# Performance work log

Measured on AMD Instinct MI355X. Metric: run time of the kernel, lower is better.

The kernel has to match this reference:

```python
import jax, jax.numpy as jnp
import numpy as np

T, D, N, W = 8192, 768, 10000, 32  # tokens, hidden dim, num spans, max span width


def setup_inputs() -> dict:
    key = jax.random.key(0)
    k1, k2, k3, k4, k5 = jax.random.split(key, 5)
    sentence_embeddings = jax.random.normal(k1, (T, D), dtype=jnp.float32)
    lengths = jax.random.randint(k2, (N,), 1, W + 1)           # span lengths in [1, W]
    starts = jax.random.randint(k3, (N,), 0, T - W)
    ends = starts + lengths - 1                                 # inclusive end, < T
    sentence_spans = jnp.stack([starts, ends], axis=1).astype(jnp.int32)
    Wq = (jax.random.normal(k4, (D, D), dtype=jnp.float32) / np.sqrt(D).astype(np.float32))
    bq = jax.random.normal(k5, (D,), dtype=jnp.float32) * 0.01
    return {"sentence_embeddings": sentence_embeddings,
            "sentence_spans": sentence_spans,
            "Wq": Wq, "bq": bq}


def reference(sentence_embeddings, sentence_spans, Wq, bq):
    # Padded + masked batched version of the per-span loop:
    #   span_emb = emb[s:e+1]; q = span_emb @ Wq.T + bq
    #   w = softmax(q @ span_emb.T, dim=1); out = (w @ span_emb).sum(0)
    starts = sentence_spans[:, 0]                               # [N]
    lengths = sentence_spans[:, 1] - starts + 1                 # inclusive end -> length
    offs = jnp.arange(W)
    pos = starts[:, None] + offs[None, :]                       # [N, W] token indices
    valid = offs[None, :] < lengths[:, None]                    # [N, W] in-span mask
    pos = jnp.clip(pos, 0, sentence_embeddings.shape[0] - 1)
    span_emb = sentence_embeddings[pos]                         # [N, W, D] ragged gather
    span_emb = jnp.where(valid[:, :, None], span_emb, 0.0)
    query = jnp.einsum('nwd,ed->nwe', span_emb, Wq) + bq        # [N, W, D]
    scores = jnp.einsum('nqd,nkd->nqk', query, span_emb)        # [N, W, W]
    scores = jnp.where(valid[:, None, :], scores, -jnp.inf)     # mask pad keys (softmax dim=1)
    weights = jax.nn.softmax(scores, axis=-1)
    attn = jnp.einsum('nqk,nkd->nqd', weights, span_emb)        # [N, W, D]
    attn = jnp.where(valid[:, :, None], attn, 0.0)              # drop pad query rows
    return attn.sum(axis=1)                                     # [N, D] == torch.sum(attention, dim=0) per span
```

## Files before the change

### kernel.cpp

```cpp
#include <hip/hip_runtime.h>
#include <hip/hip_bf16.h>
#include <cstddef>
#include <cstdint>

constexpr int Tt = 8192;
constexpr int Dd = 768;
constexpr int Nn = 10000;
constexpr int Ww = 32;

typedef __bf16 bf16x8 __attribute__((ext_vector_type(8)));
typedef __bf16 bf16x4 __attribute__((ext_vector_type(4)));
typedef _Float16 half8v __attribute__((ext_vector_type(8)));
typedef _Float16 half4v __attribute__((ext_vector_type(4)));
typedef float f32x4 __attribute__((ext_vector_type(4)));

#define MFMA16(a, b, c) __builtin_amdgcn_mfma_f32_16x16x32_bf16((a), (b), (c), 0, 0, 0)
#define MFMAH(a, b, c) __builtin_amdgcn_mfma_f32_16x16x32_f16((a), (b), (c), 0, 0, 0)

__global__ __launch_bounds__(256) void conv_f16_kernel(const float* __restrict__ emb,
                                                       const float* __restrict__ Wq,
                                                       _Float16* __restrict__ Ef,
                                                       _Float16* __restrict__ Wf) {
    const int nE = (Tt * Dd) / 4;
    const int nW = (Dd * Dd) / 4;
    const int i = blockIdx.x * 256 + threadIdx.x;
    if (i < nE) {
        const float4 v = reinterpret_cast<const float4*>(emb)[i];
        half4v o;
        o[0] = (_Float16)v.x; o[1] = (_Float16)v.y;
        o[2] = (_Float16)v.z; o[3] = (_Float16)v.w;
        reinterpret_cast<half4v*>(Ef)[i] = o;
    } else {
        const int j = i - nE;
        if (j < nW) {
            const float4 v = reinterpret_cast<const float4*>(Wq)[j];
            half4v o;
            o[0] = (_Float16)v.x; o[1] = (_Float16)v.y;
            o[2] = (_Float16)v.z; o[3] = (_Float16)v.w;
            reinterpret_cast<half4v*>(Wf)[j] = o;
        }
    }
}

template <bool LO>
__global__ __launch_bounds__(256) void conv_kernel(const float* __restrict__ src,
                                                   __bf16* __restrict__ h,
                                                   __bf16* __restrict__ l, int n4) {
    const int i = blockIdx.x * 256 + threadIdx.x;
    if (i >= n4) return;
    const float4 v = reinterpret_cast<const float4*>(src)[i];
    bf16x4 oh, ol;
    oh[0] = (__bf16)v.x; oh[1] = (__bf16)v.y; oh[2] = (__bf16)v.z; oh[3] = (__bf16)v.w;
    reinterpret_cast<bf16x4*>(h)[i] = oh;
    if (LO) {
        ol[0] = (__bf16)(v.x - (float)oh[0]);
        ol[1] = (__bf16)(v.y - (float)oh[1]);
        ol[2] = (__bf16)(v.z - (float)oh[2]);
        ol[3] = (__bf16)(v.w - (float)oh[3]);
        reinterpret_cast<bf16x4*>(l)[i] = ol;
    }
}

__global__ __launch_bounds__(256) void zero_kernel(int* __restrict__ p, int n) {
    const int i = blockIdx.x * 256 + threadIdx.x;
    if (i < n) p[i] = 0;
}

__global__ __launch_bounds__(256) void hist_kernel(const int* __restrict__ spans,
                                                   int* __restrict__ hist) {
    const int i = blockIdx.x * 256 + threadIdx.x;
    if (i < Nn) atomicAdd(&hist[spans[2 * i]], 1);
}

__global__ __launch_bounds__(256) void scan_kernel(int* __restrict__ hist) {
    __shared__ int part[256];
    const int t = threadIdx.x;
    int vals[32];
    int sum = 0;
#pragma unroll
    for (int i = 0; i < 32; ++i) { vals[i] = hist[t * 32 + i]; sum += vals[i]; }
    part[t] = sum;
    __syncthreads();
    for (int off = 1; off < 256; off <<= 1) {
        const int v = (t >= off) ? part[t - off] : 0;
        __syncthreads();
        part[t] += v;
        __syncthreads();
    }
    int run = (t == 0) ? 0 : part[t - 1];
#pragma unroll
    for (int i = 0; i < 32; ++i) { const int v = vals[i]; hist[t * 32 + i] = run; run += v; }
}

__global__ __launch_bounds__(256) void scatter_kernel(const int* __restrict__ spans,
                                                      int* __restrict__ offs,
                                                      int* __restrict__ perm) {
    const int i = blockIdx.x * 256 + threadIdx.x;
    if (i < Nn) {
        const int p = atomicAdd(&offs[spans[2 * i]], 1);
        perm[p] = i;
    }
}

template <bool SPLIT>
__global__ __launch_bounds__(256) void qproj_kernel(const float* __restrict__ emb,
                                                    const float* __restrict__ Wq,
                                                    const float* __restrict__ bq,
                                                    __bf16* __restrict__ Qh,
                                                    __bf16* __restrict__ Ql) {
    __shared__ float As[64][32];
    __shared__ float Bs[64][32];
    const int tid = threadIdx.x;
    const int tx = tid & 15;
    const int ty = tid >> 4;
    const int m0 = blockIdx.x * 64;
    const int n0 = blockIdx.y * 64;

    float acc[4][4] = {};

    for (int kc = 0; kc < Dd; kc += 32) {
#pragma unroll
        for (int i = 0; i < 2; ++i) {
            const int f   = tid + i * 256;
            const int row = f >> 3;
            const int c4  = f & 7;
            const int ph  = (c4 + (row >> 2)) & 7;
            *reinterpret_cast<float4*>(&As[row][ph * 4]) =
                *reinterpret_cast<const float4*>(&emb[(size_t)(m0 + row) * Dd + kc + c4 * 4]);
            *reinterpret_cast<float4*>(&Bs[row][ph * 4]) =
                *reinterpret_cast<const float4*>(&Wq[(size_t)(n0 + row) * Dd + kc + c4 * 4]);
        }
        __syncthreads();
#pragma unroll
        for (int d4 = 0; d4 < 8; ++d4) {
            float4 av[4], bv[4];
#pragma unroll
            for (int r = 0; r < 4; ++r)
                av[r] = *reinterpret_cast<const float4*>(&As[ty * 4 + r][((d4 + ty) & 7) * 4]);
#pragma unroll
            for (int c = 0; c < 4; ++c)
                bv[c] = *reinterpret_cast<const float4*>(&Bs[tx * 4 + c][((d4 + tx) & 7) * 4]);
#pragma unroll
            for (int r = 0; r < 4; ++r)
#pragma unroll
                for (int c = 0; c < 4; ++c) {
                    acc[r][c] += av[r].x * bv[c].x;
                    acc[r][c] += av[r].y * bv[c].y;
                    acc[r][c] += av[r].z * bv[c].z;
                    acc[r][c] += av[r].w * bv[c].w;
                }
        }
        __syncthreads();
    }
#pragma unroll
    for (int r = 0; r < 4; ++r) {
        bf16x4 oh, ol;
#pragma unroll
        for (int c = 0; c < 4; ++c) {
            const float v = acc[r][c] + bq[n0 + tx * 4 + c];
            const __bf16 h = (__bf16)v;
            oh[c] = h;
            if (SPLIT) ol[c] = (__bf16)(v - (float)h);
        }
        const size_t off = (size_t)(m0 + ty * 4 + r) * Dd + n0 + tx * 4;
        *reinterpret_cast<bf16x4*>(&Qh[off]) = oh;
        if (SPLIT) *reinterpret_cast<bf16x4*>(&Ql[off]) = ol;
    }
}

__global__ __launch_bounds__(256) void qproj_f16_kernel(const _Float16* __restrict__ Ef,
                                                        const _Float16* __restrict__ Wf,
                                                        const float* __restrict__ bq,
                                                        _Float16* __restrict__ Qf) {
    __shared__ __align__(16) _Float16 As[128 * 64];
    __shared__ __align__(16) _Float16 Bs[96 * 64];

    const int tid  = threadIdx.x;
    const int wave = tid >> 6;
    const int lane = tid & 63;

    const int b   = blockIdx.x;
    const int xcd = b & 7;
    const int li  = b >> 3;
    const int mt  = xcd * 8 + (li >> 3);
    const int nt  = li & 7;
    const int m0 = mt * 128;
    const int n0 = nt * 96;
    const int wm = (wave & 1) * 64;
    const int wn = (wave >> 1) * 48;
    const int fr = lane & 15;
    const int kg = lane >> 4;

    int ar[4], ao[4];
#pragma unroll
    for (int i = 0; i < 4; ++i) {
        const int s = tid + i * 256;
        ar[i] = s >> 3;
        ao[i] = ((s & 7) ^ (ar[i] & 7)) * 8;
    }
    int br[3], bo[3];
#pragma unroll
    for (int i = 0; i < 3; ++i) {
        const int s = tid + i * 256;
        br[i] = s >> 3;
        bo[i] = ((s & 7) ^ (br[i] & 7)) * 8;
    }

    f32x4 acc[4][3] = {};

    for (int kc = 0; kc < Dd; kc += 64) {
        half8v ra[4], rb[3];
#pragma unroll
        for (int i = 0; i < 4; ++i)
            ra[i] = *reinterpret_cast<const half8v*>(&Ef[(size_t)(m0 + ar[i]) * Dd + kc + ao[i]]);
#pragma unroll
        for (int i = 0; i < 3; ++i)
            rb[i] = *reinterpret_cast<const half8v*>(&Wf[(size_t)(n0 + br[i]) * Dd + kc + bo[i]]);
        __syncthreads();
#pragma unroll
        for (int i = 0; i < 4; ++i)
            *reinterpret_cast<half8v*>(&As[(tid + i * 256) * 8]) = ra[i];
#pragma unroll
        for (int i = 0; i < 3; ++i)
            *reinterpret_cast<half8v*>(&Bs[(tid + i * 256) * 8]) = rb[i];
        __syncthreads();

#pragma unroll
        for (int step = 0; step < 2; ++step) {
            const int g = kg + 4 * step;
            half8v a[4], bb[3];
#pragma unroll
            for (int r = 0; r < 4; ++r) {
                const int R = wm + r * 16 + fr;
                a[r] = *reinterpret_cast<const half8v*>(&As[R * 64 + (g ^ (R & 7)) * 8]);
            }
#pragma unroll
            for (int c = 0; c < 3; ++c) {
                const int R = wn + c * 16 + fr;
                bb[c] = *reinterpret_cast<const half8v*>(&Bs[R * 64 + (g ^ (R & 7)) * 8]);
            }
#pragma unroll
            for (int r = 0; r < 4; ++r)
#pragma unroll
                for (int c = 0; c < 3; ++c)
                    acc[r][c] = MFMAH(a[r], bb[c], acc[r][c]);
        }
    }

#pragma unroll
    for (int c = 0; c < 3; ++c) {
        const int ocol = n0 + wn + c * 16 + fr;
        const float bqv = bq[ocol];
#pragma unroll
        for (int r = 0; r < 4; ++r)
#pragma unroll
            for (int j = 0; j < 4; ++j) {
                const int orow = m0 + wm + r * 16 + kg * 4 + j;
                Qf[(size_t)orow * Dd + ocol] = (_Float16)(acc[r][c][j] + bqv);
            }
    }
}

__global__ __launch_bounds__(256) void span_attn_win_kernel(const _Float16* __restrict__ Ef,
                                                            const int* __restrict__ spans,
                                                            const _Float16* __restrict__ Qf,
                                                            const int* __restrict__ perm,
                                                            float* __restrict__ out) {
    constexpr int WR = 48, CH = 128, ST = 136, NCH = Dd / CH;
    __shared__ __align__(16) _Float16 Qs[WR * ST];
    __shared__ __align__(16) _Float16 Es[WR * ST];

    const int tid  = threadIdx.x;
    const int wave = tid >> 6;
    const int lane = tid & 63;

    const int b     = blockIdx.x;
    const int bp    = (b & 7) * 313 + (b >> 3);
    const int slot0 = bp * 4;
    const int slot  = slot0 + wave;
    const bool active = slot < Nn;

    int s0 = perm[slot0 < Nn ? slot0 : (Nn - 1)];
    if ((unsigned)s0 >= (unsigned)Nn) s0 = 0;
    int s = active ? perm[slot] : s0;
    if ((unsigned)s >= (unsigned)Nn) s = 0;

    const int w0    = spans[2 * s0];
    const int start = spans[2 * s];
    const int L     = spans[2 * s + 1] - start + 1;
    const bool big  = L > 16;
    const int sl    = start - w0;
    const bool inwin = active && sl >= 0 && sl <= (WR - 32);

    const int row = lane & 15;
    const int kq  = lane >> 4;

    const size_t gq = (size_t)(start + row) * Dd + kq * 8;

    f32x4 acc00 = {0.f, 0.f, 0.f, 0.f};
    f32x4 acc01 = {0.f, 0.f, 0.f, 0.f};
    f32x4 acc10 = {0.f, 0.f, 0.f, 0.f};
    f32x4 acc11 = {0.f, 0.f, 0.f, 0.f};

    for (int c = 0; c < NCH; ++c) {
        const int c0 = c * CH;
        __syncthreads();
#pragma unroll
        for (int i = 0; i < 3; ++i) {
            const int seg = tid + i * 256;
            const int r  = seg >> 4;
            const int cs = seg & 15;
            const int gr = w0 + r < Tt ? w0 + r : Tt - 1;
            const size_t ga = (size_t)gr * Dd + c0 + cs * 8;
            *reinterpret_cast<half8v*>(&Qs[r * ST + cs * 8]) =
                *reinterpret_cast<const half8v*>(&Qf[ga]);
            *reinterpret_cast<half8v*>(&Es[r * ST + cs * 8]) =
                *reinterpret_cast<const half8v*>(&Ef[ga]);
        }
        __syncthreads();

        if (inwin) {
            const int ab = (sl + row) * ST + kq * 8;
#pragma unroll
            for (int j = 0; j < 4; ++j) {
                const int o = j * 32;
                const half8v a0 = *reinterpret_cast<const half8v*>(&Qs[ab + o]);
                const half8v b0 = *reinterpret_cast<const half8v*>(&Es[ab + o]);
                acc00 = MFMAH(a0, b0, acc00);
                if (big) {
                    const half8v a1 = *reinterpret_cast<const half8v*>(&Qs[ab + 16 * ST + o]);
                    const half8v b1 = *reinterpret_cast<const half8v*>(&Es[ab + 16 * ST + o]);
                    acc01 = MFMAH(a0, b1, acc01);
                    acc10 = MFMAH(a1, b0, acc10);
                    acc11 = MFMAH(a1, b1, acc11);
                }
            }
        } else if (active) {
#pragma unroll
            for (int j = 0; j < 4; ++j) {
                const int o = c0 + j * 32;
                const half8v a0 = *reinterpret_cast<const half8v*>(&Qf[gq + o]);
                const half8v b0 = *reinterpret_cast<const half8v*>(&Ef[gq + o]);
                acc00 = MFMAH(a0, b0, acc00);
                if (big) {
                    const half8v a1 = *reinterpret_cast<const half8v*>(&Qf[gq + 16 * Dd + o]);
                    const half8v b1 = *reinterpret_cast<const half8v*>(&Ef[gq + 16 * Dd + o]);
                    acc01 = MFMAH(a0, b1, acc01);
                    acc10 = MFMAH(a1, b0, acc10);
                    acc11 = MFMAH(a1, b1, acc11);
                }
            }
        }
    }

    const float NEG = -1e30f;
    const bool kv0 = row < L;
    const bool kv1 = (16 + row) < L;
    float cA, cB;
    {
        float w00[4], w01[4], w10[4], w11[4];
#pragma unroll
        for (int r = 0; r < 4; ++r) {
            float m = kv0 ? acc00[r] : NEG;
            if (big) m = fmaxf(m, kv1 ? acc01[r] : NEG);
#pragma unroll
            for (int st = 1; st <= 8; st <<= 1) m = fmaxf(m, __shfl_xor(m, st));
            const float e0 = kv0 ? __expf(acc00[r] - m) : 0.f;
            const float e1 = (big && kv1) ? __expf(acc01[r] - m) : 0.f;
            float sum = e0 + e1;
#pragma unroll
            for (int st = 1; st <= 8; st <<= 1) sum += __shfl_xor(sum, st);
            const float inv = 1.f / sum;
            const bool qv = (kq * 4 + r) < L;
            w00[r] = qv ? e0 * inv : 0.f;
            w01[r] = qv ? e1 * inv : 0.f;
            if (big) {
                float mh = kv0 ? acc10[r] : NEG;
                mh = fmaxf(mh, kv1 ? acc11[r] : NEG);
#pragma unroll
                for (int st = 1; st <= 8; st <<= 1) mh = fmaxf(mh, __shfl_xor(mh, st));
                const float f0 = kv0 ? __expf(acc10[r] - mh) : 0.f;
                const float f1 = kv1 ? __expf(acc11[r] - mh) : 0.f;
                float sh = f0 + f1;
#pragma unroll
                for (int st = 1; st <= 8; st <<= 1) sh += __shfl_xor(sh, st);
                const float invh = 1.f / sh;
                const bool qvh = (16 + kq * 4 + r) < L;
                w10[r] = qvh ? f0 * invh : 0.f;
                w11[r] = qvh ? f1 * invh : 0.f;
            }
        }
        float pa = w00[0] + w00[1] + w00[2] + w00[3];
        float pb = 0.f;
        if (big) {
            pa += w10[0] + w10[1] + w10[2] + w10[3];
            pb = w01[0] + w01[1] + w01[2] + w01[3] +
                 w11[0] + w11[1] + w11[2] + w11[3];
        }
        pa += __shfl_xor(pa, 16);
        pa += __shfl_xor(pa, 32);
        if (big) {
            pb += __shfl_xor(pb, 16);
            pb += __shfl_xor(pb, 32);
        }
        cA = pa;
        cB = pb;
    }

    if (active) {
        f32x4 o[3] = {};
        const int KP = (L + 3) & ~3;
        const _Float16* ebase = Ef + (size_t)start * Dd + lane * 4;
        for (int k = 0; k < KP; k += 4) {
            float cv[4];
            half4v ev[4][3];
#pragma unroll
            for (int j = 0; j < 4; ++j) {
                const int kk = k + j;
                cv[j] = (kk < 16) ? __shfl(cA, kk) : __shfl(cB, kk - 16);
#pragma unroll
                for (int i = 0; i < 3; ++i)
                    ev[j][i] = *reinterpret_cast<const half4v*>(ebase + (size_t)kk * Dd + i * 256);
            }
#pragma unroll
            for (int j = 0; j < 4; ++j)
#pragma unroll
                for (int i = 0; i < 3; ++i) {
                    o[i][0] += cv[j] * (float)ev[j][i][0];
                    o[i][1] += cv[j] * (float)ev[j][i][1];
                    o[i][2] += cv[j] * (float)ev[j][i][2];
                    o[i][3] += cv[j] * (float)ev[j][i][3];
                }
        }
#pragma unroll
        for (int i = 0; i < 3; ++i)
            *reinterpret_cast<f32x4*>(&out[(size_t)s * Dd + i * 256 + lane * 4]) = o[i];
    }
}

template <bool SPLIT, bool SORTED>
__global__ __launch_bounds__(256) void span_attn_g_kernel(const __bf16* __restrict__ Eb,
                                                          const int* __restrict__ spans,
                                                          const __bf16* __restrict__ Qh,
                                                          const __bf16* __restrict__ Ql,
                                                          const int* __restrict__ perm,
                                                          float* __restrict__ out) {
    const int wave = threadIdx.x >> 6;
    const int lane = threadIdx.x & 63;

    int s;
    bool active;
    if (SORTED) {
        const int b    = blockIdx.x;
        const int bp   = (b & 7) * 313 + (b >> 3);
        const int slot = bp * 4 + wave;
        active = slot < Nn;
        int sv = active ? perm[slot] : 0;
        if ((unsigned)sv >= (unsigned)Nn) sv = 0;
        s = sv;
    } else {
        s = blockIdx.x * 4 + wave;
        active = true;
    }

    const int start = spans[2 * s];
    const int L     = spans[2 * s + 1] - start + 1;
    const bool big  = L > 16;

    const int row = lane & 15;
    const int kq  = lane >> 4;

    const size_t rbase = (size_t)(start + row) * Dd + kq * 8;
    const __bf16* qh0 = Qh + rbase;
    const __bf16* eb0 = Eb + rbase;
    const __bf16* ql0 = SPLIT ? (Ql + rbase) : nullptr;

    f32x4 acc00 = {0.f, 0.f, 0.f, 0.f};
    f32x4 acc01 = {0.f, 0.f, 0.f, 0.f};
    f32x4 acc10 = {0.f, 0.f, 0.f, 0.f};
    f32x4 acc11 = {0.f, 0.f, 0.f, 0.f};

    if (!big) {
        for (int kc = 0; kc < Dd; kc += 128) {
            bf16x8 A[4], B[4], AL[4];
#pragma unroll
            for (int j = 0; j < 4; ++j) {
                const int o = kc + j * 32;
                A[j] = *reinterpret_cast<const bf16x8*>(qh0 + o);
                B[j] = *reinterpret_cast<const bf16x8*>(eb0 + o);
                if (SPLIT) AL[j] = *reinterpret_cast<const bf16x8*>(ql0 + o);
            }
#pragma unroll
            for (int j = 0; j < 4; ++j) {
                acc00 = MFMA16(A[j], B[j], acc00);
                if (SPLIT) acc00 = MFMA16(AL[j], B[j], acc00);
            }
        }
    } else {
        for (int kc = 0; kc < Dd; kc += 64) {
            bf16x8 A0[2], A1[2], B0[2], B1[2], AL0[2], AL1[2];
#pragma unroll
            for (int j = 0; j < 2; ++j) {
                const int o = kc + j * 32;
                A0[j] = *reinterpret_cast<const bf16x8*>(qh0 + o);
                A1[j] = *reinterpret_cast<const bf16x8*>(qh0 + 16 * Dd + o);
                B0[j] = *reinterpret_cast<const bf16x8*>(eb0 + o);
                B1[j] = *reinterpret_cast<const bf16x8*>(eb0 + 16 * Dd + o);
                if (SPLIT) {
                    AL0[j] = *reinterpret_cast<const bf16x8*>(ql0 + o);
                    AL1[j] = *reinterpret_cast<const bf16x8*>(ql0 + 16 * Dd + o);
                }
            }
#pragma unroll
            for (int j = 0; j < 2; ++j) {
                acc00 = MFMA16(A0[j], B0[j], acc00);
                acc01 = MFMA16(A0[j], B1[j], acc01);
                acc10 = MFMA16(A1[j], B0[j], acc10);
                acc11 = MFMA16(A1[j], B1[j], acc11);
                if (SPLIT) {
                    acc00 = MFMA16(AL0[j], B0[j], acc00);
                    acc01 = MFMA16(AL0[j], B1[j], acc01);
                    acc10 = MFMA16(AL1[j], B0[j], acc10);
                    acc11 = MFMA16(AL1[j], B1[j], acc11);
                }
            }
        }
    }

    const float NEG = -1e30f;
    const bool kv0 = row < L;
    const bool kv1 = (16 + row) < L;
    float cA, cB;
    {
        float w00[4], w01[4], w10[4], w11[4];
#pragma unroll
        for (int r = 0; r < 4; ++r) {
            float m = kv0 ? acc00[r] : NEG;
            if (big) m = fmaxf(m, kv1 ? acc01[r] : NEG);
#pragma unroll
            for (int st = 1; st <= 8; st <<= 1) m = fmaxf(m, __shfl_xor(m, st));
            const float e0 = kv0 ? __expf(acc00[r] - m) : 0.f;
            const float e1 = (big && kv1) ? __expf(acc01[r] - m) : 0.f;
            float sum = e0 + e1;
#pragma unroll
            for (int st = 1; st <= 8; st <<= 1) sum += __shfl_xor(sum, st);
            const float inv = 1.f / sum;
            const bool qv = (kq * 4 + r) < L;
            w00[r] = qv ? e0 * inv : 0.f;
            w01[r] = qv ? e1 * inv : 0.f;
            if (big) {
                float mh = kv0 ? acc10[r] : NEG;
                mh = fmaxf(mh, kv1 ? acc11[r] : NEG);
#pragma unroll
                for (int st = 1; st <= 8; st <<= 1) mh = fmaxf(mh, __shfl_xor(mh, st));
                const float f0 = kv0 ? __expf(acc10[r] - mh) : 0.f;
                const float f1 = kv1 ? __expf(acc11[r] - mh) : 0.f;
                float sh = f0 + f1;
#pragma unroll
                for (int st = 1; st <= 8; st <<= 1) sh += __shfl_xor(sh, st);
                const float invh = 1.f / sh;
                const bool qvh = (16 + kq * 4 + r) < L;
                w10[r] = qvh ? f0 * invh : 0.f;
                w11[r] = qvh ? f1 * invh : 0.f;
            }
        }
        float pa = w00[0] + w00[1] + w00[2] + w00[3];
        float pb = 0.f;
        if (big) {
            pa += w10[0] + w10[1] + w10[2] + w10[3];
            pb = w01[0] + w01[1] + w01[2] + w01[3] +
                 w11[0] + w11[1] + w11[2] + w11[3];
        }
        pa += __shfl_xor(pa, 16);
        pa += __shfl_xor(pa, 32);
        if (big) {
            pb += __shfl_xor(pb, 16);
            pb += __shfl_xor(pb, 32);
        }
        cA = pa;
        cB = pb;
    }

    if (active) {
        f32x4 o[3] = {};
        const int KP = (L + 3) & ~3;
        const __bf16* ebase = Eb + (size_t)start * Dd + lane * 4;
        for (int k = 0; k < KP; k += 4) {
            float cv[4];
            bf16x4 ev[4][3];
#pragma unroll
            for (int j = 0; j < 4; ++j) {
                const int kk = k + j;
                cv[j] = (kk < 16) ? __shfl(cA, kk) : __shfl(cB, kk - 16);
#pragma unroll
                for (int i = 0; i < 3; ++i)
                    ev[j][i] = *reinterpret_cast<const bf16x4*>(ebase + (size_t)kk * Dd + i * 256);
            }
#pragma unroll
            for (int j = 0; j < 4; ++j)
#pragma unroll
                for (int i = 0; i < 3; ++i) {
                    o[i][0] += cv[j] * (float)ev[j][i][0];
                    o[i][1] += cv[j] * (float)ev[j][i][1];
                    o[i][2] += cv[j] * (float)ev[j][i][2];
                    o[i][3] += cv[j] * (float)ev[j][i][3];
                }
        }
#pragma unroll
        for (int i = 0; i < 3; ++i)
            *reinterpret_cast<f32x4*>(&out[(size_t)s * Dd + i * 256 + lane * 4]) = o[i];
    }
}

extern "C" void kernel_launch(void* const* d_in, const int* in_sizes, int n_in,
                              void* d_out, int out_size, void* d_ws, size_t ws_size,
                              hipStream_t stream) {
    const float* emb   = (const float*)d_in[0];
    const int*   spans = (const int*)d_in[1];
    const float* Wq    = (const float*)d_in[2];
    const float* bq    = (const float*)d_in[3];
    float*       out   = (float*)d_out;

    const size_t TD = (size_t)Tt * Dd;
    const size_t DD = (size_t)Dd * Dd;
    const size_t intBytes = (size_t)(8192 + 10016) * sizeof(int);
    auto align16 = [](size_t x) { return (x + 15) & ~(size_t)15; };

    const size_t needMain = align16((2 * TD + DD) * 2) + intBytes;
    const size_t needB = align16(3 * TD * 2) + intBytes;
    const size_t needC = 3 * TD * 2;

    if (ws_size >= needMain) {
        char* base = (char*)d_ws;
        _Float16* Qf = (_Float16*)base;
        _Float16* Ef = (_Float16*)(base + TD * 2);
        _Float16* Wf = (_Float16*)(base + 2 * TD * 2);
        int* hist = (int*)(base + align16((2 * TD + DD) * 2));
        int* perm = hist + 8192;

        const int convBlocks = (int)((TD / 4 + DD / 4) / 256);
        conv_f16_kernel<<<convBlocks, 256, 0, stream>>>(emb, Wq, Ef, Wf);
        zero_kernel<<<32, 256, 0, stream>>>(hist, 8192);
        hist_kernel<<<40, 256, 0, stream>>>(spans, hist);
        scan_kernel<<<1, 256, 0, stream>>>(hist);
        scatter_kernel<<<40, 256, 0, stream>>>(spans, hist, perm);
        qproj_f16_kernel<<<512, 256, 0, stream>>>(Ef, Wf, bq, Qf);
        span_attn_win_kernel<<<2504, 256, 0, stream>>>(Ef, spans, Qf, perm, out);
    } else if (ws_size >= needB) {
        __bf16* w = (__bf16*)d_ws;
        __bf16* Qh = w;
        __bf16* Ql = w + TD;
        __bf16* Eh = w + 2 * TD;
        int* hist = (int*)((char*)d_ws + align16(3 * TD * 2));
        int* perm = hist + 8192;

        conv_kernel<false><<<(int)(TD / 4 / 256), 256, 0, stream>>>(emb, Eh, nullptr, (int)(TD / 4));
        zero_kernel<<<32, 256, 0, stream>>>(hist, 8192);
        hist_kernel<<<40, 256, 0, stream>>>(spans, hist);
        scan_kernel<<<1, 256, 0, stream>>>(hist);
        scatter_kernel<<<40, 256, 0, stream>>>(spans, hist, perm);
        qproj_kernel<true><<<dim3(Tt / 64, Dd / 64), 256, 0, stream>>>(emb, Wq, bq, Qh, Ql);
        span_attn_g_kernel<true, true><<<2504, 256, 0, stream>>>(Eh, spans, Qh, Ql, perm, out);
    } else if (ws_size >= needC) {
        __bf16* w = (__bf16*)d_ws;
        __bf16* Qh = w;
        __bf16* Ql = w + TD;
        __bf16* Eh = w + 2 * TD;
        conv_kernel<false><<<(int)(TD / 4 / 256), 256, 0, stream>>>(emb, Eh, nullptr, (int)(TD / 4));
        qproj_kernel<true><<<dim3(Tt / 64, Dd / 64), 256, 0, stream>>>(emb, Wq, bq, Qh, Ql);
        span_attn_g_kernel<true, false><<<2500, 256, 0, stream>>>(Eh, spans, Qh, Ql, nullptr, out);
    } else {
        __bf16* w = (__bf16*)d_ws;
        __bf16* Qh = w;
        __bf16* Eh = w + TD;
        conv_kernel<false><<<(int)(TD / 4 / 256), 256, 0, stream>>>(emb, Eh, nullptr, (int)(TD / 4));
        qproj_kernel<false><<<dim3(Tt / 64, Dd / 64), 256, 0, stream>>>(emb, Wq, bq, Qh, nullptr);
        span_attn_g_kernel<false, false><<<2500, 256, 0, stream>>>(Eh, spans, Qh, nullptr, nullptr, out);
    }
}
```

Measured before the change: 152.6 us.

## Process two sorted spans per wave and register-prefetch next window chunk

Each block now handles 8 sorted spans (two per wave) instead of 4, so each shared-memory window of Q and E rows is reused by more spans, and the grid is halved to 1250 blocks with a new XCD-aware block remap. The next 128-column chunk is loaded into registers while the current chunk is being consumed, which overlaps global loads with MFMA work. The cost is more registers per thread (two accumulator sets plus prefetch buffers) and fewer blocks, which may lower occupancy and parallelism. The active guard was also removed, so correctness relies on 1250*8 exactly covering N.

```diff
diff --git a/kernel.cpp b/kernel.cpp
--- a/kernel.cpp
+++ b/kernel.cpp
@@ -274,167 +274,199 @@
     const int wave = tid >> 6;
     const int lane = tid & 63;
 
-    const int b     = blockIdx.x;
-    const int bp    = (b & 7) * 313 + (b >> 3);
-    const int slot0 = bp * 4;
-    const int slot  = slot0 + wave;
-    const bool active = slot < Nn;
-
-    int s0 = perm[slot0 < Nn ? slot0 : (Nn - 1)];
+    const int b   = blockIdx.x;
+    const int xcd = b & 7;
+    const int li  = b >> 3;
+    const int bp  = (xcd < 2) ? xcd * 157 + li : 314 + (xcd - 2) * 156 + li;
+    const int slot0 = bp * 8;
+
+    int s0 = perm[slot0];
     if ((unsigned)s0 >= (unsigned)Nn) s0 = 0;
-    int s = active ? perm[slot] : s0;
-    if ((unsigned)s >= (unsigned)Nn) s = 0;
-
-    const int w0    = spans[2 * s0];
-    const int start = spans[2 * s];
-    const int L     = spans[2 * s + 1] - start + 1;
-    const bool big  = L > 16;
-    const int sl    = start - w0;
-    const bool inwin = active && sl >= 0 && sl <= (WR - 32);
+    const int w0 = spans[2 * s0];
 
     const int row = lane & 15;
     const int kq  = lane >> 4;
 
-    const size_t gq = (size_t)(start + row) * Dd + kq * 8;
-
-    f32x4 acc00 = {0.f, 0.f, 0.f, 0.f};
-    f32x4 acc01 = {0.f, 0.f, 0.f, 0.f};
-    f32x4 acc10 = {0.f, 0.f, 0.f, 0.f};
-    f32x4 acc11 = {0.f, 0.f, 0.f, 0.f};
+    int  sS[2], stS[2], LS[2];
+    bool bigS[2], inwS[2];
+#pragma unroll
+    for (int sp = 0; sp < 2; ++sp) {
+        int s = perm[slot0 + wave * 2 + sp];
+        if ((unsigned)s >= (unsigned)Nn) s = 0;
+        sS[sp]   = s;
+        stS[sp]  = spans[2 * s];
+        LS[sp]   = spans[2 * s + 1] - stS[sp] + 1;
+        bigS[sp] = LS[sp] > 16;
+        const int sl = stS[sp] - w0;
+        inwS[sp] = (sl >= 0) && (sl <= (WR - 32));
+    }
+
+    int    ldso[3];
+    size_t gbo[3];
+#pragma unroll
+    for (int i = 0; i < 3; ++i) {
+        const int seg = tid + i * 256;
+        const int r   = seg >> 4;
+        const int cs  = seg & 15;
+        ldso[i] = r * ST + cs * 8;
+        const int gr = (w0 + r < Tt) ? (w0 + r) : (Tt - 1);
+        gbo[i] = (size_t)gr * Dd + cs * 8;
+    }
+
+    f32x4 acc[2][4] = {};
+
+    half8v rq[3], re[3];
+#pragma unroll
+    for (int i = 0; i < 3; ++i) {
+        rq[i] = *reinterpret_cast<const half8v*>(&Qf[gbo[i]]);
+        re[i] = *reinterpret_cast<const half8v*>(&Ef[gbo[i]]);
+    }
 
     for (int c = 0; c < NCH; ++c) {
+        __syncthreads();
+#pragma unroll
+        for (int i = 0; i < 3; ++i) {
+            *reinterpret_cast<half8v*>(&Qs[ldso[i]]) = rq[i];
+            *reinterpret_cast<half8v*>(&Es[ldso[i]]) = re[i];
+        }
+        __syncthreads();
+
+        if (c + 1 < NCH) {
+            const size_t cb = (size_t)(c + 1) * CH;
+#pragma unroll
+            for (int i = 0; i < 3; ++i) {
+                rq[i] = *reinterpret_cast<const half8v*>(&Qf[gbo[i] + cb]);
+                re[i] = *reinterpret_cast<const half8v*>(&Ef[gbo[i] + cb]);
+            }
+        }
+
         const int c0 = c * CH;
-        __syncthreads();
-#pragma unroll
-        for (int i = 0; i < 3; ++i) {
-            const int seg = tid + i * 256;
-            const int r  = seg >> 4;
-            const int cs = seg & 15;
-            const int gr = w0 + r < Tt ? w0 + r : Tt - 1;
-            const size_t ga = (size_t)gr * Dd + c0 + cs * 8;
-            *reinterpret_cast<half8v*>(&Qs[r * ST + cs * 8]) =
-                *reinterpret_cast<const half8v*>(&Qf[ga]);
-            *reinterpret_cast<half8v*>(&Es[r * ST + cs * 8]) =
-                *reinterpret_cast<const half8v*>(&Ef[ga]);
-        }
-        __syncthreads();
-
-        if (inwin) {
-            const int ab = (sl + row) * ST + kq * 8;
-#pragma unroll
-            for (int j = 0; j < 4; ++j) {
-                const int o = j * 32;
-                const half8v a0 = *reinterpret_cast<const half8v*>(&Qs[ab + o]);
-                const half8v b0 = *reinterpret_cast<const half8v*>(&Es[ab + o]);
-                acc00 = MFMAH(a0, b0, acc00);
+#pragma unroll
+        for (int sp = 0; sp < 2; ++sp) {
+            const bool big = bigS[sp];
+            if (inwS[sp]) {
+                const int ab = (stS[sp] - w0 + row) * ST + kq * 8;
+#pragma unroll
+                for (int j = 0; j < 4; ++j) {
+                    const int o = j * 32;
+                    const half8v a0 = *reinterpret_cast<const half8v*>(&Qs[ab + o]);
+                    const half8v b0 = *reinterpret_cast<const half8v*>(&Es[ab + o]);
+                    acc[sp][0] = MFMAH(a0, b0, acc[sp][0]);
+                    if (big) {
+                        const half8v a1 = *reinterpret_cast<const half8v*>(&Qs[ab + 16 * ST + o]);
+                        const half8v b1 = *reinterpret_cast<const half8v*>(&Es[ab + 16 * ST + o]);
+                        acc[sp][1] = MFMAH(a0, b1, acc[sp][1]);
+                        acc[sp][2] = MFMAH(a1, b0, acc[sp][2]);
+                        acc[sp][3] = MFMAH(a1, b1, acc[sp][3]);
+                    }
+                }
+            } else {
+                const size_t gq = (size_t)(stS[sp] + row) * Dd + kq * 8;
+#pragma unroll
+                for (int j = 0; j < 4; ++j) {
+                    const int o = c0 + j * 32;
+                    const half8v a0 = *reinterpret_cast<const half8v*>(&Qf[gq + o]);
+                    const half8v b0 = *reinterpret_cast<const half8v*>(&Ef[gq + o]);
+                    acc[sp][0] = MFMAH(a0, b0, acc[sp][0]);
+                    if (big) {
+                        const half8v a1 = *reinterpret_cast<const half8v*>(&Qf[gq + 16 * Dd + o]);
+                        const half8v b1 = *reinterpret_cast<const half8v*>(&Ef[gq + 16 * Dd + o]);
+                        acc[sp][1] = MFMAH(a0, b1, acc[sp][1]);
+                        acc[sp][2] = MFMAH(a1, b0, acc[sp][2]);
+                        acc[sp][3] = MFMAH(a1, b1, acc[sp][3]);
+                    }
+                }
+            }
+        }
+    }
+
+#pragma unroll
+    for (int sp = 0; sp < 2; ++sp) {
+        const int  L   = LS[sp];
+        const bool big = bigS[sp];
+        const float NEG = -1e30f;
+        const bool kv0 = row < L;
+        const bool kv1 = (16 + row) < L;
+        float cA, cB;
+        {
+            float w00[4], w01[4], w10[4], w11[4];
+#pragma unroll
+            for (int r = 0; r < 4; ++r) {
+                float m = kv0 ? acc[sp][0][r] : NEG;
+                if (big) m = fmaxf(m, kv1 ? acc[sp][1][r] : NEG);
+#pragma unroll
+                for (int st = 1; st <= 8; st <<= 1) m = fmaxf(m, __shfl_xor(m, st));
+                const float e0 = kv0 ? __expf(acc[sp][0][r] - m) : 0.f;
+                const float e1 = (big && kv1) ? __expf(acc[sp][1][r] - m) : 0.f;
+                float sum = e0 + e1;
+#pragma unroll
+                for (int st = 1; st <= 8; st <<= 1) sum += __shfl_xor(sum, st);
+                const float inv = 1.f / sum;
+                const bool qv = (kq * 4 + r) < L;
+                w00[r] = qv ? e0 * inv : 0.f;
+                w01[r] = qv ? e1 * inv : 0.f;
                 if (big) {
-                    const half8v a1 = *reinterpret_cast<const half8v*>(&Qs[ab + 16 * ST + o]);
-                    const half8v b1 = *reinterpret_cast<const half8v*>(&Es[ab + 16 * ST + o]);
-                    acc01 = MFMAH(a0, b1, acc01);
-                    acc10 = MFMAH(a1, b0, acc10);
-                    acc11 = MFMAH(a1, b1, acc11);
+                    float mh = kv0 ? acc[sp][2][r] : NEG;
+                    mh = fmaxf(mh, kv1 ? acc[sp][3][r] : NEG);
+#pragma unroll
+                    for (int st = 1; st <= 8; st <<= 1) mh = fmaxf(mh, __shfl_xor(mh, st));
+                    const float f0 = kv0 ? __expf(acc[sp][2][r] - mh) : 0.f;
+                    const float f1 = kv1 ? __expf(acc[sp][3][r] - mh) : 0.f;
+                    float sh = f0 + f1;
+#pragma unroll
+                    for (int st = 1; st <= 8; st <<= 1) sh += __shfl_xor(sh, st);
+                    const float invh = 1.f / sh;
+                    const bool qvh = (16 + kq * 4 + r) < L;
+                    w10[r] = qvh ? f0 * invh : 0.f;
+                    w11[r] = qvh ? f1 * invh : 0.f;
                 }
             }
-        } else if (active) {
-#pragma unroll
-            for (int j = 0; j < 4; ++j) {
-                const int o = c0 + j * 32;
-                const half8v a0 = *reinterpret_cast<const half8v*>(&Qf[gq + o]);
-                const half8v b0 = *reinterpret_cast<const half8v*>(&Ef[gq + o]);
-                acc00 = MFMAH(a0, b0, acc00);
-                if (big) {
-                    const half8v a1 = *reinterpret_cast<const half8v*>(&Qf[gq + 16 * Dd + o]);
-                    const half8v b1 = *reinterpret_cast<const half8v*>(&Ef[gq + 16 * Dd + o]);
-                    acc01 = MFMAH(a0, b1, acc01);
-                    acc10 = MFMAH(a1, b0, acc10);
-                    acc11 = MFMAH(a1, b1, acc11);
+            float pa = w00[0] + w00[1] + w00[2] + w00[3];
+            float pb = 0.f;
+            if (big) {
+                pa += w10[0] + w10[1] + w10[2] + w10[3];
+                pb = w01[0] + w01[1] + w01[2] + w01[3] +
+                     w11[0] + w11[1] + w11[2] + w11[3];
+            }
+            pa += __shfl_xor(pa, 16);
+            pa += __shfl_xor(pa, 32);
+            if (big) {
+                pb += __shfl_xor(pb, 16);
+                pb += __shfl_xor(pb, 32);
+            }
+            cA = pa;
+            cB = pb;
+        }
+
+        {
+            f32x4 o[3] = {};
+            const int KP = (L + 3) & ~3;
+            const _Float16* ebase = Ef + (size_t)stS[sp] * Dd + lane * 4;
+            for (int k = 0; k < KP; k += 4) {
+                float cv[4];
+                half4v ev[4][3];
+#pragma unroll
+                for (int j = 0; j < 4; ++j) {
+                    const int kk = k + j;
+                    cv[j] = (kk < 16) ? __shfl(cA, kk) : __shfl(cB, kk - 16);
+#pragma unroll
+                    for (int i = 0; i < 3; ++i)
+                        ev[j][i] = *reinterpret_cast<const half4v*>(ebase + (size_t)kk * Dd + i * 256);
                 }
-            }
-        }
-    }
-
-    const float NEG = -1e30f;
-    const bool kv0 = row < L;
-    const bool kv1 = (16 + row) < L;
-    float cA, cB;
-    {
-        float w00[4], w01[4], w10[4], w11[4];
-#pragma unroll
-        for (int r = 0; r < 4; ++r) {
-            float m = kv0 ? acc00[r] : NEG;
-            if (big) m = fmaxf(m, kv1 ? acc01[r] : NEG);
-#pragma unroll
-            for (int st = 1; st <= 8; st <<= 1) m = fmaxf(m, __shfl_xor(m, st));
-            const float e0 = kv0 ? __expf(acc00[r] - m) : 0.f;
-            const float e1 = (big && kv1) ? __expf(acc01[r] - m) : 0.f;
-            float sum = e0 + e1;
-#pragma unroll
-            for (int st = 1; st <= 8; st <<= 1) sum += __shfl_xor(sum, st);
-            const float inv = 1.f / sum;
-            const bool qv = (kq * 4 + r) < L;
-            w00[r] = qv ? e0 * inv : 0.f;
-            w01[r] = qv ? e1 * inv : 0.f;
-            if (big) {
-                float mh = kv0 ? acc10[r] : NEG;
-                mh = fmaxf(mh, kv1 ? acc11[r] : NEG);
-#pragma unroll
-                for (int st = 1; st <= 8; st <<= 1) mh = fmaxf(mh, __shfl_xor(mh, st));
-                const float f0 = kv0 ? __expf(acc10[r] - mh) : 0.f;
-                const float f1 = kv1 ? __expf(acc11[r] - mh) : 0.f;
-                float sh = f0 + f1;
-#pragma unroll
-                for (int st = 1; st <= 8; st <<= 1) sh += __shfl_xor(sh, st);
-                const float invh = 1.f / sh;
-                const bool qvh = (16 + kq * 4 + r) < L;
-                w10[r] = qvh ? f0 * invh : 0.f;
-                w11[r] = qvh ? f1 * invh : 0.f;
-            }
-        }
-        float pa = w00[0] + w00[1] + w00[2] + w00[3];
-        float pb = 0.f;
-        if (big) {
-            pa += w10[0] + w10[1] + w10[2] + w10[3];
-            pb = w01[0] + w01[1] + w01[2] + w01[3] +
-                 w11[0] + w11[1] + w11[2] + w11[3];
-        }
-        pa += __shfl_xor(pa, 16);
-        pa += __shfl_xor(pa, 32);
-        if (big) {
-            pb += __shfl_xor(pb, 16);
-            pb += __shfl_xor(pb, 32);
-        }
-        cA = pa;
-        cB = pb;
-    }
-
-    if (active) {
-        f32x4 o[3] = {};
-        const int KP = (L + 3) & ~3;
-        const _Float16* ebase = Ef + (size_t)start * Dd + lane * 4;
-        for (int k = 0; k < KP; k += 4) {
-            float cv[4];
-            half4v ev[4][3];
-#pragma unroll
-            for (int j = 0; j < 4; ++j) {
-                const int kk = k + j;
-                cv[j] = (kk < 16) ? __shfl(cA, kk) : __shfl(cB, kk - 16);
-#pragma unroll
-                for (int i = 0; i < 3; ++i)
-                    ev[j][i] = *reinterpret_cast<const half4v*>(ebase + (size_t)kk * Dd + i * 256);
-            }
-#pragma unroll
-            for (int j = 0; j < 4; ++j)
-#pragma unroll
-                for (int i = 0; i < 3; ++i) {
-                    o[i][0] += cv[j] * (float)ev[j][i][0];
-                    o[i][1] += cv[j] * (float)ev[j][i][1];
-                    o[i][2] += cv[j] * (float)ev[j][i][2];
-                    o[i][3] += cv[j] * (float)ev[j][i][3];
-                }
-        }
-#pragma unroll
-        for (int i = 0; i < 3; ++i)
-            *reinterpret_cast<f32x4*>(&out[(size_t)s * Dd + i * 256 + lane * 4]) = o[i];
+#pragma unroll
+                for (int j = 0; j < 4; ++j)
+#pragma unroll
+                    for (int i = 0; i < 3; ++i) {
+                        o[i][0] += cv[j] * (float)ev[j][i][0];
+                        o[i][1] += cv[j] * (float)ev[j][i][1];
+                        o[i][2] += cv[j] * (float)ev[j][i][2];
+                        o[i][3] += cv[j] * (float)ev[j][i][3];
+                    }
+            }
+#pragma unroll
+            for (int i = 0; i < 3; ++i)
+                *reinterpret_cast<f32x4*>(&out[(size_t)sS[sp] * Dd + i * 256 + lane * 4]) = o[i];
+        }
     }
 }
 
@@ -645,7 +677,7 @@
         scan_kernel<<<1, 256, 0, stream>>>(hist);
         scatter_kernel<<<40, 256, 0, stream>>>(spans, hist, perm);
         qproj_f16_kernel<<<512, 256, 0, stream>>>(Ef, Wf, bq, Qf);
-        span_attn_win_kernel<<<2504, 256, 0, stream>>>(Ef, spans, Qf, perm, out);
+        span_attn_win_kernel<<<1250, 256, 0, stream>>>(Ef, spans, Qf, perm, out);
     } else if (ws_size >= needB) {
         __bf16* w = (__bf16*)d_ws;
         __bf16* Qh = w;
```

New measurement: 175.8 us. 15.2% more time.
